# Optimization experiments

Hardware: AMD Instinct MI355X
Metric: run time of the kernel (lower is better)

Reference implementation:

```python
import jax, jax.numpy as jnp
import numpy as np
from jax import lax
import math

N_QUBITS = 10
N_LAYERS = 4
PI = jnp.float32(math.pi)


def _c(x):
    return x.astype(jnp.complex64)


def rx_mat(t):
    c = _c(jnp.cos(0.5 * t)); s = _c(jnp.sin(0.5 * t))
    return jnp.stack([jnp.stack([c, -1j * s]), jnp.stack([-1j * s, c])])


def ry_mat(t):
    c = _c(jnp.cos(0.5 * t)); s = _c(jnp.sin(0.5 * t))
    return jnp.stack([jnp.stack([c, -s]), jnp.stack([s, c])])


def rz_mat(t):
    e0 = jnp.exp(_c(jnp.zeros_like(t)) - 0.5j * _c(t))
    e1 = jnp.exp(0.5j * _c(t))
    z = jnp.zeros_like(e0)
    return jnp.stack([jnp.stack([e0, z]), jnp.stack([z, e1])])


def apply_1q(psi, U, q):
    # psi: (2,)*n complex, apply 2x2 U on axis q
    psi = jnp.moveaxis(psi, q, 0)
    psi = jnp.tensordot(U, psi, axes=(1, 0))
    return jnp.moveaxis(psi, 0, q)


def apply_cnot(psi, ctrl, tgt):
    psi = jnp.moveaxis(psi, (ctrl, tgt), (0, 1))
    a00, a01, a10, a11 = psi[0, 0], psi[0, 1], psi[1, 0], psi[1, 1]
    psi = jnp.stack([jnp.stack([a00, a01]), jnp.stack([a11, a10])])
    return jnp.moveaxis(psi, (0, 1), (ctrl, tgt))


def vqc(state, weights):
    # state: (D,) float32 angles; weights: (layers, n, 3)
    n, L = N_QUBITS, N_LAYERS
    D = state.shape[0]
    psi = jnp.full((2,) * n, 2.0 ** (-n / 2.0), dtype=jnp.complex64)  # H^n |0>
    for layer in range(L):
        for q in range(n):
            ang = state[(layer * n + q) % D]
            psi = apply_1q(psi, rx_mat(ang), q)
            psi = apply_1q(psi, ry_mat(ang), q)
            psi = apply_1q(psi, rz_mat(weights[layer, q, 0]), q)
            psi = apply_1q(psi, ry_mat(weights[layer, q, 1]), q)
            psi = apply_1q(psi, rz_mat(weights[layer, q, 2]), q)
        for q in range(n - 1):
            psi = apply_cnot(psi, q, q + 1)
        psi = apply_cnot(psi, n - 1, 0)
    probs = jnp.real(psi * jnp.conj(psi))  # (2,)*n
    zdiag = jnp.array([1.0, -1.0], dtype=jnp.float32)
    exps = [jnp.sum(probs * zdiag.reshape((1,) * q + (2,) + (1,) * (n - q - 1)))
            for q in range(n)]
    return jnp.stack(exps)  # (n,)


def lstm_forward(x, W_ih, W_hh, b_ih, b_hh):
    # x: [B,T,Din]; PyTorch gate order: i, f, g, o
    B, T, _ = x.shape
    H = W_hh.shape[1]
    b = b_ih + b_hh

    def step(carry, xt):
        h, c = carry
        gates = xt @ W_ih.T + h @ W_hh.T + b
        i, f, g, o = jnp.split(gates, 4, axis=-1)
        i = jax.nn.sigmoid(i); f = jax.nn.sigmoid(f)
        g = jnp.tanh(g); o = jax.nn.sigmoid(o)
        c = f * c + i * g
        h = o * jnp.tanh(c)
        return (h, c), h

    h0 = jnp.zeros((B, H), x.dtype)
    c0 = jnp.zeros((B, H), x.dtype)
    _, hs = lax.scan(step, (h0, c0), jnp.swapaxes(x, 0, 1))
    return jnp.swapaxes(hs, 0, 1)  # [B,T,H]


def _forward(s, lstm_s, W_ih, W_hh, b_ih, b_hh, proj_W, proj_b,
             in_proj_W, in_proj_b, out_proj_W, out_proj_b,
             qweights, W1, b1, W2, b2):
    hs = lstm_forward(lstm_s, W_ih, W_hh, b_ih, b_hh)      # [B,T,H]
    lstm_last = hs[:, -1, :]                               # [B,H]
    state_full = jnp.concatenate([lstm_last, s], axis=1)   # [B,E]
    lstm_proj = hs @ proj_W.T + proj_b                     # [B,T,E]
    E = proj_W.shape[0]
    Wq, Wk, Wv = in_proj_W[:E], in_proj_W[E:2 * E], in_proj_W[2 * E:]
    bq, bk, bv = in_proj_b[:E], in_proj_b[E:2 * E], in_proj_b[2 * E:]
    q = state_full @ Wq.T + bq                             # [B,E] (1 query token)
    k = lstm_proj @ Wk.T + bk                              # [B,T,E]
    v = lstm_proj @ Wv.T + bv
    scale = 1.0 / jnp.sqrt(jnp.float32(E))                 # num_heads=1 -> head_dim=E
    attn = jax.nn.softmax(jnp.einsum('be,bte->bt', q, k) * scale, axis=-1)
    ctx = jnp.einsum('bt,bte->be', attn, v)
    attn_out = ctx @ out_proj_W.T + out_proj_b             # [B,E]
    merged_state = jnp.concatenate([attn_out, s], axis=1)  # [B,E+F]
    state_norm = jnp.tanh(merged_state) * PI
    qfeat = jax.vmap(lambda st: vqc(st, qweights))(state_norm)  # [B,n]
    merged = jnp.concatenate([merged_state, qfeat], axis=1)
    x = jax.nn.relu(merged @ W1.T + b1)
    return x @ W2.T + b2


def setup_inputs() -> dict:
    key = jax.random.key(0)
    ks = jax.random.split(key, 16)
    B, T = 512, 256
    Din, H, F = 128, 256, 64
    E = H + F          # 320 = state_dim
    Dm = E + F         # 384 = merged_state dim
    n_l1, n_act = 512, 8

    def g(k, shape, std):
        return (std * jax.random.normal(k, shape)).astype(jnp.float32)

    return {
        's': jax.random.normal(ks[0], (B, F), jnp.float32),
        'lstm_s': jax.random.normal(ks[1], (B, T, Din), jnp.float32),
        'W_ih': g(ks[2], (4 * H, Din), 0.05),
        'W_hh': g(ks[3], (4 * H, H), 0.05),
        'b_ih': jnp.zeros((4 * H,), jnp.float32),
        'b_hh': jnp.zeros((4 * H,), jnp.float32),
        'proj_W': g(ks[4], (E, H), 0.05),
        'proj_b': 0.1 * jnp.ones((E,), jnp.float32),
        'in_proj_W': g(ks[5], (3 * E, E), 0.05),
        'in_proj_b': jnp.zeros((3 * E,), jnp.float32),
        'out_proj_W': g(ks[6], (E, E), 0.05),
        'out_proj_b': jnp.zeros((E,), jnp.float32),
        'qweights': jax.random.uniform(ks[7], (N_LAYERS, N_QUBITS, 3), jnp.float32, 0.0, 2.0 * math.pi),
        'W1': g(ks[8], (n_l1, Dm + N_QUBITS), 0.05),
        'b1': 0.1 * jnp.ones((n_l1,), jnp.float32),
        'W2': g(ks[9], (n_act, n_l1), 0.05),
        'b2': 0.1 * jnp.ones((n_act,), jnp.float32),
    }


def reference(s, lstm_s, W_ih, W_hh, b_ih, b_hh, proj_W, proj_b,
              in_proj_W, in_proj_b, out_proj_W, out_proj_b,
              qweights, W1, b1, W2, b2):
    return _forward(s, lstm_s, W_ih, W_hh, b_ih, b_hh, proj_W, proj_b,
                    in_proj_W, in_proj_b, out_proj_W, out_proj_b,
                    qweights, W1, b1, W2, b2)
```

## Files before the change

### kernel.cpp

```cpp
#include <hip/hip_runtime.h>
#include <hip/hip_bf16.h>
#include <math.h>

typedef unsigned int u32;
typedef unsigned long long u64;
typedef unsigned short u16;
typedef __attribute__((ext_vector_type(8))) short short8;
typedef __attribute__((ext_vector_type(4))) float f32x4;
typedef __attribute__((ext_vector_type(4))) int v4i;

#define PI_F 3.14159265358979f
#define B_   512
#define T_   256
#define DIN  128
#define H_   256
#define G4   1024
#define F_   64
#define E_   320
#define DM   384
#define NL1  512
#define NACT 8
#define KMLP 394

__device__ v4i llvm_amdgcn_raw_buffer_load_v4i32(v4i rsrc, int voffset,
                                                 int soffset, int aux)
    __asm("llvm.amdgcn.raw.buffer.load.v4i32");
__device__ void llvm_amdgcn_raw_buffer_store_i32(int vdata, v4i rsrc,
                                                 int voffset, int soffset,
                                                 int aux)
    __asm("llvm.amdgcn.raw.buffer.store.i32");

__device__ __forceinline__ v4i make_srd(const void* p) {
  v4i r;
  r.x = (int)(u32)(u64)p;
  r.y = (int)(u32)((u64)p >> 32);
  r.z = (int)0xFFFFFFFFu;
  r.w = 0x00020000;
  return r;
}

__device__ __forceinline__ float b2f(u16 h) {
  union { u32 u; float f; } v; v.u = ((u32)h) << 16; return v.f;
}
__device__ __forceinline__ u16 f2b(float f) {
  union { float f; u32 u; } v; v.f = f;
  u32 r = (v.u + 0x7FFFu + ((v.u >> 16) & 1u)) >> 16;
  return (u16)r;
}
__device__ __forceinline__ float sigf(float x) { return 1.0f / (1.0f + __expf(-x)); }
__device__ __forceinline__ float tanhfast(float x) { return 2.0f / (1.0f + __expf(-2.0f * x)) - 1.0f; }
__device__ __forceinline__ float2 cmul(float2 a, float2 b) {
  return make_float2(a.x * b.x - a.y * b.y, a.x * b.y + a.y * b.x);
}
__device__ __forceinline__ float2 cadd(float2 a, float2 b) {
  return make_float2(a.x + b.x, a.y + b.y);
}

__global__ void k_prep1(const float* __restrict__ lstm_s,
                        const float* __restrict__ W_ih,
                        const float* __restrict__ W_hh,
                        const float* __restrict__ b_ih,
                        const float* __restrict__ b_hh,
                        const float* __restrict__ ipw,
                        const float* __restrict__ ipb,
                        const float* __restrict__ projb,
                        const float* __restrict__ qw,
                        const float* __restrict__ W1,
                        u16* __restrict__ xbf,
                        u16* __restrict__ hs,
                        u16* __restrict__ Wg,
                        float* __restrict__ bb,
                        float* __restrict__ W1t,
                        float* __restrict__ uw,
                        float* __restrict__ bkp,
                        float* __restrict__ bvp,
                        u32* __restrict__ cnt) {
  const int bid = blockIdx.x;
  const int tid = threadIdx.x;
  if (bid < 8192) {
    u32 u = (u32)bid * 256u + tid;
    u32 c8 = u & 15u, b = (u >> 4) & 511u, t = u >> 13;
    const float* src = lstm_s + ((size_t)b * T_ + t) * DIN + c8 * 8;
    union { u16 h[8]; uint4 v; } tmp;
#pragma unroll
    for (int i = 0; i < 8; ++i) tmp.h[i] = f2b(src[i]);
    *(uint4*)(xbf + ((size_t)t * B_ + b) * DIN + c8 * 8) = tmp.v;
  } else if (bid < 8384) {
    u32 u = (u32)(bid - 8192) * 256u + tid;
    u32 c8 = u % 48u, r = u / 48u;
    const float* src = (c8 < 16) ? (W_ih + (size_t)r * DIN + c8 * 8)
                                 : (W_hh + (size_t)r * H_ + (c8 - 16) * 8);
    union { u16 h[8]; uint4 v; } tmp;
#pragma unroll
    for (int i = 0; i < 8; ++i) tmp.h[i] = f2b(src[i]);
    *(uint4*)(Wg + (size_t)r * 384 + c8 * 8) = tmp.v;
  } else if (bid < 8448) {
    u32 u = (u32)(bid - 8384) * 256u + tid;
    ((uint4*)hs)[u] = make_uint4(0, 0, 0, 0);
  } else if (bid < 9236) {
    u32 u = (u32)(bid - 8448) * 256u + tid;
    u32 k = u / 512u, nn = u % 512u;
    W1t[u] = W1[(size_t)nn * KMLP + k];
  } else if (bid == 9236) {
    for (int i = tid; i < 1024; i += 256) bb[i] = b_ih[i] + b_hh[i];
    for (int i = tid; i < 1024; i += 256) cnt[i] = 0u;
    if (tid < 40) {
      float w0 = qw[tid * 3 + 0], w1 = qw[tid * 3 + 1], w2 = qw[tid * 3 + 2];
      float c0 = cosf(0.5f * w0), s0 = sinf(0.5f * w0);
      float c1 = cosf(0.5f * w1), s1 = sinf(0.5f * w1);
      float c2 = cosf(0.5f * w2), s2 = sinf(0.5f * w2);
      float2 e0m = make_float2(c0, -s0), e0p = make_float2(c0, s0);
      float2 e2m = make_float2(c2, -s2), e2p = make_float2(c2, s2);
      float2 t00 = make_float2(c1 * e0m.x, c1 * e0m.y);
      float2 t01 = make_float2(-s1 * e0p.x, -s1 * e0p.y);
      float2 t10 = make_float2(s1 * e0m.x, s1 * e0m.y);
      float2 t11 = make_float2(c1 * e0p.x, c1 * e0p.y);
      float2 u00 = cmul(e2m, t00), u01 = cmul(e2m, t01);
      float2 u10 = cmul(e2p, t10), u11 = cmul(e2p, t11);
      float* o = uw + tid * 8;
      o[0] = u00.x; o[1] = u00.y; o[2] = u01.x; o[3] = u01.y;
      o[4] = u10.x; o[5] = u10.y; o[6] = u11.x; o[7] = u11.y;
    }
  } else if (bid <= 9238) {
    int o = (bid - 9237) * 256 + tid;
    if (o < E_) {
      float acc = ipb[E_ + o];
      for (int e = 0; e < E_; ++e) acc += ipw[(size_t)(E_ + o) * E_ + e] * projb[e];
      bkp[o] = acc;
    }
  } else {
    int o = (bid - 9239) * 256 + tid;
    if (o < E_) {
      float acc = ipb[2 * E_ + o];
      for (int e = 0; e < E_; ++e) acc += ipw[(size_t)(2 * E_ + o) * E_ + e] * projb[e];
      bvp[o] = acc;
    }
  }
}

__global__ void k_prep2(const float* __restrict__ ipw, const float* __restrict__ projW,
                        float* __restrict__ Wkp, float* __restrict__ Wvp) {
  int bid = blockIdx.x, tid = threadIdx.x;
  int o = (bid < 320) ? bid : (bid - 320);
  const float* wrow = ipw + (size_t)((bid < 320 ? E_ : 2 * E_) + o) * E_;
  float acc = 0.f;
  for (int e = 0; e < E_; ++e) acc += wrow[e] * projW[(size_t)e * H_ + tid];
  (bid < 320 ? Wkp : Wvp)[(size_t)o * H_ + tid] = acc;
}

__global__ void k_prep3(const float* __restrict__ ipw, const float* __restrict__ ipb,
                        const float* __restrict__ opw, const float* __restrict__ opb,
                        const float* __restrict__ Wkp, const float* __restrict__ Wvp,
                        const float* __restrict__ bkp, const float* __restrict__ bvp,
                        float* __restrict__ WuT, float* __restrict__ bu,
                        float* __restrict__ wd, float* __restrict__ ddp,
                        float* __restrict__ Wovt, float* __restrict__ bov) {
  int bid = blockIdx.x, tid = threadIdx.x;
  if (bid < 320) {
    int e = bid;
    float acc = 0.f;
    for (int o = 0; o < E_; ++o) acc += Wkp[(size_t)o * H_ + tid] * ipw[(size_t)o * E_ + e];
    WuT[(size_t)e * H_ + tid] = acc;
  } else if (bid < 576) {
    int jj = bid - 320;
    for (int i = tid; i < E_; i += 256) {
      float acc = 0.f;
      for (int o = 0; o < E_; ++o) acc += opw[(size_t)i * E_ + o] * Wvp[(size_t)o * H_ + jj];
      Wovt[(size_t)jj * E_ + i] = acc;
    }
  } else {
    {
      float acc = 0.f;
      for (int o = 0; o < E_; ++o) acc += Wkp[(size_t)o * H_ + tid] * ipb[o];
      bu[tid] = acc;
    }
    for (int idx = tid; idx < E_; idx += 256) {
      float a1 = 0.f, a2 = opb[idx];
      for (int o = 0; o < E_; ++o) {
        a1 += ipw[(size_t)o * E_ + idx] * bkp[o];
        a2 += opw[(size_t)idx * E_ + o] * bvp[o];
      }
      wd[idx] = a1; bov[idx] = a2;
    }
    if (tid == 0) {
      float acc = 0.f;
      for (int o = 0; o < E_; ++o) acc += ipb[o] * bkp[o];
      ddp[0] = acc;
    }
  }
}

struct LstmArgs {
  const u16* xbf; u16* hs; const u16* Wg; const float* bb; u32* cnt;
};

__launch_bounds__(256, 1)
__global__ void k_lstm(LstmArgs A) {
  const int g   = blockIdx.x & 7;
  const int n   = blockIdx.x >> 3;
  const int tid = threadIdx.x;
  const int wid = tid >> 6, lane = tid & 63;
  __shared__ __align__(16) u16 Wl[32 * 392];

  for (int idx = tid; idx < 32 * 48; idx += 256) {
    int ln = idx / 48, c8 = idx % 48;
    int gr = (ln >> 3) * 256 + n * 8 + (ln & 7);
    *(uint4*)&Wl[ln * 392 + c8 * 8] = *(const uint4*)&A.Wg[(size_t)gr * 384 + c8 * 8];
  }
  const int j  = lane & 7;
  const int gc = n * 8 + j;
  const float bbi = A.bb[gc], bbf2 = A.bb[256 + gc];
  const float bbg = A.bb[512 + gc], bbo = A.bb[768 + gc];

  const int quad = lane >> 4;
  const int mrow = lane & 15;
  const int brow = g * 64 + wid * 16 + mrow;
  const int erow0 = g * 64 + wid * 16 + quad * 4;
  const bool hi = (lane & 8) != 0;
  float crs[4] = {0.f, 0.f, 0.f, 0.f};
  u32* mycnt = A.cnt + g * 64;
  u32 target = 0;

  const v4i hs_srd = make_srd(A.hs);
  const int hvoff = (brow * H_ + quad * 8) * 2;

  uint4 xc0, xc1, xc2, xc3, xn0, xn1, xn2, xn3;
  {
    const u16* xb = A.xbf + ((size_t)0 * B_ + brow) * DIN + quad * 8;
    xc0 = *(const uint4*)(xb + 0);
    xc1 = *(const uint4*)(xb + 32);
    xc2 = *(const uint4*)(xb + 64);
    xc3 = *(const uint4*)(xb + 96);
  }
  __syncthreads();

  for (int t = 0; t < T_; ++t) {
    const int hsoff = t * (B_ * H_ * 2);
    uint4 h0 = __builtin_bit_cast(uint4, llvm_amdgcn_raw_buffer_load_v4i32(hs_srd, hvoff +   0, hsoff, 17));
    uint4 h1 = __builtin_bit_cast(uint4, llvm_amdgcn_raw_buffer_load_v4i32(hs_srd, hvoff +  64, hsoff, 17));
    uint4 h2 = __builtin_bit_cast(uint4, llvm_amdgcn_raw_buffer_load_v4i32(hs_srd, hvoff + 128, hsoff, 17));
    uint4 h3 = __builtin_bit_cast(uint4, llvm_amdgcn_raw_buffer_load_v4i32(hs_srd, hvoff + 192, hsoff, 17));
    uint4 h4 = __builtin_bit_cast(uint4, llvm_amdgcn_raw_buffer_load_v4i32(hs_srd, hvoff + 256, hsoff, 17));
    uint4 h5 = __builtin_bit_cast(uint4, llvm_amdgcn_raw_buffer_load_v4i32(hs_srd, hvoff + 320, hsoff, 17));
    uint4 h6 = __builtin_bit_cast(uint4, llvm_amdgcn_raw_buffer_load_v4i32(hs_srd, hvoff + 384, hsoff, 17));
    uint4 h7 = __builtin_bit_cast(uint4, llvm_amdgcn_raw_buffer_load_v4i32(hs_srd, hvoff + 448, hsoff, 17));
    {
      const int tn = (t + 1 < T_) ? (t + 1) : t;
      const u16* xb = A.xbf + ((size_t)tn * B_ + brow) * DIN + quad * 8;
      xn0 = *(const uint4*)(xb + 0);
      xn1 = *(const uint4*)(xb + 32);
      xn2 = *(const uint4*)(xb + 64);
      xn3 = *(const uint4*)(xb + 96);
    }

    f32x4 acc0 = {0.f, 0.f, 0.f, 0.f}, acc1 = {0.f, 0.f, 0.f, 0.f};
#define MMSTEP(AV, KOFF)                                                          \
    {                                                                             \
      short8 av  = __builtin_bit_cast(short8, AV);                                \
      short8 bv0 = __builtin_bit_cast(short8,                                     \
          *(const uint4*)&Wl[mrow * 392 + (KOFF) + quad * 8]);                    \
      short8 bv1 = __builtin_bit_cast(short8,                                     \
          *(const uint4*)&Wl[(16 + mrow) * 392 + (KOFF) + quad * 8]);             \
      acc0 = __builtin_amdgcn_mfma_f32_16x16x32_bf16(av, bv0, acc0, 0, 0, 0);     \
      acc1 = __builtin_amdgcn_mfma_f32_16x16x32_bf16(av, bv1, acc1, 0, 0, 0);     \
    }
    MMSTEP(xc0, 0)   MMSTEP(xc1, 32)  MMSTEP(xc2, 64)  MMSTEP(xc3, 96)
    MMSTEP(h0, 128)  MMSTEP(h1, 160)  MMSTEP(h2, 192)  MMSTEP(h3, 224)
    MMSTEP(h4, 256)  MMSTEP(h5, 288)  MMSTEP(h6, 320)  MMSTEP(h7, 352)
#undef MMSTEP

    const int hsoff_o = (t + 1) * (B_ * H_ * 2);
#pragma unroll
    for (int r = 0; r < 4; ++r) {
      float x0 = acc0[r], x1v = acc1[r];
      float y0 = __shfl_xor(x0, 8, 64);
      float y1 = __shfl_xor(x1v, 8, 64);
      float iv = (hi ? y0 : x0) + bbi;
      float fv = (hi ? x0 : y0) + bbf2;
      float gv = (hi ? y1 : x1v) + bbg;
      float ov = (hi ? x1v : y1) + bbo;
      float cc = sigf(fv) * crs[r] + sigf(iv) * tanhfast(gv);
      crs[r] = cc;
      float hh = sigf(ov) * tanhfast(cc);
      float hh2 = __shfl_xor(hh, 1, 64);
      if (!hi && ((j & 1) == 0)) {
        u32 pk = (u32)f2b(hh) | ((u32)f2b(hh2) << 16);
        llvm_amdgcn_raw_buffer_store_i32((int)pk, hs_srd,
                                         ((erow0 + r) * H_ + gc) * 2, hsoff_o, 17);
      }
    }
    target += 32;
    if (t != T_ - 1) {
      __syncthreads();
      if (tid == 0) {
        __hip_atomic_fetch_add(mycnt, 1u, __ATOMIC_RELAXED, __HIP_MEMORY_SCOPE_AGENT);
        int guard = 0;
        while (__hip_atomic_load(mycnt, __ATOMIC_RELAXED, __HIP_MEMORY_SCOPE_AGENT) < target) {
          __builtin_amdgcn_s_sleep(1);
          if (++guard > (1 << 24)) break;
        }
      }
      __syncthreads();
      xc0 = xn0; xc1 = xn1; xc2 = xn2; xc3 = xn3;
    }
  }
}

__global__ void k_u(const u16* __restrict__ hs, const float* __restrict__ s,
                    const float* __restrict__ WuT, const float* __restrict__ bu,
                    const float* __restrict__ wd, const float* __restrict__ ddp,
                    float* __restrict__ u, float* __restrict__ dvec) {
  int b = blockIdx.x, tid = threadIdx.x;
  __shared__ float z[E_];
  __shared__ float red[256];
  z[tid] = b2f(hs[((size_t)T_ * B_ + b) * H_ + tid]);
  if (tid < F_) z[H_ + tid] = s[(size_t)b * F_ + tid];
  __syncthreads();
  float acc = bu[tid];
  for (int e = 0; e < E_; ++e) acc += WuT[(size_t)e * H_ + tid] * z[e];
  u[(size_t)b * H_ + tid] = acc;
  float p = 0.f;
  for (int e = tid; e < E_; e += 256) p += wd[e] * z[e];
  red[tid] = p;
  __syncthreads();
  for (int s2 = 128; s2 > 0; s2 >>= 1) {
    if (tid < s2) red[tid] += red[tid + s2];
    __syncthreads();
  }
  if (tid == 0) dvec[b] = red[0] + ddp[0];
}

__global__ void k_aw(const u16* __restrict__ hs, const float* __restrict__ u,
                     const float* __restrict__ dvec, float* __restrict__ wv) {
  int b = blockIdx.x, tid = threadIdx.x;
  int wid = tid >> 6, lane = tid & 63;
  __shared__ float sc[T_];
  __shared__ float red[256];
  const float db = dvec[b];
  const float scale = 0.055901699437494745f;
  float4 ul = *(const float4*)&u[(size_t)b * H_ + lane * 4];
  for (int tt = 0; tt < 64; ++tt) {
    int t = wid * 64 + tt;
    u32 rw0 = ((const u32*)(hs + ((size_t)(t + 1) * B_ + b) * H_))[lane * 2];
    u32 rw1 = ((const u32*)(hs + ((size_t)(t + 1) * B_ + b) * H_))[lane * 2 + 1];
    union { u32 uu; float f; } f0, f1, f2, f3;
    f0.uu = rw0 << 16; f1.uu = rw0 & 0xFFFF0000u;
    f2.uu = rw1 << 16; f3.uu = rw1 & 0xFFFF0000u;
    float p = f0.f * ul.x + f1.f * ul.y + f2.f * ul.z + f3.f * ul.w;
#pragma unroll
    for (int off = 32; off > 0; off >>= 1) p += __shfl_xor(p, off, 64);
    if (lane == 0) sc[t] = (p + db) * scale;
  }
  __syncthreads();
  float v = sc[tid];
  red[tid] = v;
  __syncthreads();
  for (int s2 = 128; s2 > 0; s2 >>= 1) {
    if (tid < s2) red[tid] = fmaxf(red[tid], red[tid + s2]);
    __syncthreads();
  }
  float m = red[0];
  __syncthreads();
  float e = __expf(v - m);
  red[tid] = e;
  __syncthreads();
  for (int s2 = 128; s2 > 0; s2 >>= 1) {
    if (tid < s2) red[tid] += red[tid + s2];
    __syncthreads();
  }
  float inv = 1.f / red[0];
  __syncthreads();
  sc[tid] = e * inv;
  __syncthreads();
  float acc = 0.f;
#pragma unroll 8
  for (int t = 0; t < T_; ++t) {
    acc += sc[t] * b2f(hs[((size_t)(t + 1) * B_ + b) * H_ + tid]);
  }
  wv[(size_t)b * H_ + tid] = acc;
}

__global__ void k_ao(const float* __restrict__ wv, const float* __restrict__ Wovt,
                     const float* __restrict__ bov, const float* __restrict__ s,
                     float* __restrict__ mst) {
  int b = blockIdx.x, tid = threadIdx.x;
  __shared__ float wl[H_];
  if (tid < H_) wl[tid] = wv[(size_t)b * H_ + tid];
  __syncthreads();
  if (tid < E_) {
    float acc = bov[tid];
    for (int jj = 0; jj < H_; ++jj) acc += Wovt[(size_t)jj * E_ + tid] * wl[jj];
    mst[(size_t)b * DM + tid] = acc;
  } else if (tid < DM) {
    mst[(size_t)b * DM + tid] = s[(size_t)b * F_ + (tid - E_)];
  }
}

__global__ void k_vqc(const float* __restrict__ mst, const float* __restrict__ uwg,
                      float* __restrict__ qf) {
  int b = blockIdx.x, tid = threadIdx.x;
  __shared__ float2 psi[1024];
  __shared__ float ang[40];
  __shared__ float uwl[320];
  __shared__ float part[4][10];
  if (tid < 40) ang[tid] = tanhf(mst[(size_t)b * DM + tid]) * PI_F;
  uwl[tid] = uwg[tid];
  if (tid < 64) uwl[256 + tid] = uwg[256 + tid];
#pragma unroll
  for (int k = 0; k < 4; ++k) psi[tid + k * 256] = make_float2(0.03125f, 0.f);
  __syncthreads();
  for (int l = 0; l < 4; ++l) {
    for (int q = 0; q < 10; ++q) {
      int lq = l * 10 + q;
      float a = ang[lq];
      float ca = __cosf(0.5f * a), sa = __sinf(0.5f * a);
      float cs = ca * sa;
      float2 m00 = make_float2(ca * ca, sa * sa);
      float2 m01 = make_float2(-cs, -cs);
      float2 m10 = make_float2(cs, -cs);
      float2 m11 = make_float2(ca * ca, -sa * sa);
      const float* uwp = &uwl[lq * 8];
      float2 a00 = make_float2(uwp[0], uwp[1]), a01 = make_float2(uwp[2], uwp[3]);
      float2 a10 = make_float2(uwp[4], uwp[5]), a11 = make_float2(uwp[6], uwp[7]);
      float2 u00 = cadd(cmul(a00, m00), cmul(a01, m10));
      float2 u01 = cadd(cmul(a00, m01), cmul(a01, m11));
      float2 u10 = cadd(cmul(a10, m00), cmul(a11, m10));
      float2 u11 = cadd(cmul(a10, m01), cmul(a11, m11));
      int bp = 9 - q;
      __syncthreads();
#pragma unroll
      for (int k = 0; k < 2; ++k) {
        int p = tid + k * 256;
        int i0 = ((p >> bp) << (bp + 1)) | (p & ((1 << bp) - 1));
        int i1 = i0 | (1 << bp);
        float2 A0 = psi[i0], A1 = psi[i1];
        psi[i0] = cadd(cmul(u00, A0), cmul(u01, A1));
        psi[i1] = cadd(cmul(u10, A0), cmul(u11, A1));
      }
    }
    for (int q = 0; q < 9; ++q) {
      int lo = 8 - q;
      __syncthreads();
      int p = tid;
      int i0 = ((p >> lo) << (lo + 2)) | (2 << lo) | (p & ((1 << lo) - 1));
      int i1 = i0 | (1 << lo);
      float2 tmp = psi[i0]; psi[i0] = psi[i1]; psi[i1] = tmp;
    }
    __syncthreads();
    {
      int i0 = (tid << 1) | 1;
      int i1 = i0 | 512;
      float2 tmp = psi[i0]; psi[i0] = psi[i1]; psi[i1] = tmp;
    }
  }
  __syncthreads();
  float acc[10];
#pragma unroll
  for (int q = 0; q < 10; ++q) acc[q] = 0.f;
#pragma unroll
  for (int k = 0; k < 4; ++k) {
    int idx = tid + k * 256;
    float2 A = psi[idx];
    float pr = A.x * A.x + A.y * A.y;
#pragma unroll
    for (int q = 0; q < 10; ++q) acc[q] += ((idx >> (9 - q)) & 1) ? -pr : pr;
  }
  int lane = tid & 63, wid = tid >> 6;
#pragma unroll
  for (int q = 0; q < 10; ++q) {
    float vq = acc[q];
#pragma unroll
    for (int off = 32; off > 0; off >>= 1) vq += __shfl_xor(vq, off, 64);
    if (lane == 0) part[wid][q] = vq;
  }
  __syncthreads();
  if (tid < 10) qf[(size_t)b * 10 + tid] = part[0][tid] + part[1][tid] + part[2][tid] + part[3][tid];
}

__global__ void k_mlp(const float* __restrict__ mst, const float* __restrict__ qf,
                      const float* __restrict__ W1t, const float* __restrict__ b1,
                      const float* __restrict__ W2, const float* __restrict__ b2,
                      float* __restrict__ out) {
  int b = blockIdx.x, tid = threadIdx.x;
  __shared__ float mg[KMLP];
  __shared__ float x1[NL1];
  __shared__ float red[256];
  for (int i = tid; i < DM; i += 256) mg[i] = mst[(size_t)b * DM + i];
  if (tid < 10) mg[DM + tid] = qf[(size_t)b * 10 + tid];
  __syncthreads();
#pragma unroll
  for (int hh = 0; hh < 2; ++hh) {
    int nn = tid + hh * 256;
    float acc = b1[nn];
#pragma unroll 4
    for (int k = 0; k < KMLP; ++k) acc += W1t[(size_t)k * NL1 + nn] * mg[k];
    x1[nn] = fmaxf(acc, 0.f);
  }
  __syncthreads();
  int a = tid >> 5, l32 = tid & 31;
  float p = 0.f;
  for (int k = l32; k < NL1; k += 32) p += x1[k] * W2[(size_t)a * NL1 + k];
  red[tid] = p;
  __syncthreads();
  if (tid < 8) {
    float acc = b2[tid];
#pragma unroll
    for (int i = 0; i < 32; ++i) acc += red[tid * 32 + i];
    out[(size_t)b * NACT + tid] = acc;
  }
}

extern "C" void kernel_launch(void* const* d_in, const int* in_sizes, int n_in,
                              void* d_out, int out_size, void* d_ws, size_t ws_size,
                              hipStream_t stream) {
  const float* s      = (const float*)d_in[0];
  const float* lstm_s = (const float*)d_in[1];
  const float* W_ih   = (const float*)d_in[2];
  const float* W_hh   = (const float*)d_in[3];
  const float* b_ih   = (const float*)d_in[4];
  const float* b_hh   = (const float*)d_in[5];
  const float* projW  = (const float*)d_in[6];
  const float* projb  = (const float*)d_in[7];
  const float* ipw    = (const float*)d_in[8];
  const float* ipb    = (const float*)d_in[9];
  const float* opw    = (const float*)d_in[10];
  const float* opb    = (const float*)d_in[11];
  const float* qw     = (const float*)d_in[12];
  const float* W1     = (const float*)d_in[13];
  const float* b1     = (const float*)d_in[14];
  const float* W2     = (const float*)d_in[15];
  const float* b2     = (const float*)d_in[16];
  float* out = (float*)d_out;

  char* wsb = (char*)d_ws;
  size_t off = 0;
  auto alloc = [&](size_t bytes) -> void* {
    void* p = wsb + off;
    off = (off + bytes + 255) & ~(size_t)255;
    return p;
  };
  u16*  xbf  = (u16*)alloc((size_t)T_ * B_ * DIN * 2);
  u16*  hs   = (u16*)alloc((size_t)(T_ + 1) * B_ * H_ * 2);
  u16*  Wg   = (u16*)alloc((size_t)G4 * 384 * 2);
  float* bb  = (float*)alloc(G4 * 4);
  float* Wkp = (float*)alloc((size_t)E_ * H_ * 4);
  float* Wvp = (float*)alloc((size_t)E_ * H_ * 4);
  float* bkp = (float*)alloc(E_ * 4);
  float* bvp = (float*)alloc(E_ * 4);
  float* WuT = (float*)alloc((size_t)E_ * H_ * 4);
  float* bu  = (float*)alloc(H_ * 4);
  float* wd  = (float*)alloc(E_ * 4);
  float* ddp = (float*)alloc(256);
  float* Wovt= (float*)alloc((size_t)H_ * E_ * 4);
  float* bov = (float*)alloc(E_ * 4);
  float* uu  = (float*)alloc((size_t)B_ * H_ * 4);
  float* dvec= (float*)alloc(B_ * 4);
  float* wv  = (float*)alloc((size_t)B_ * H_ * 4);
  float* mst = (float*)alloc((size_t)B_ * DM * 4);
  float* qf  = (float*)alloc((size_t)B_ * 10 * 4);
  float* uw  = (float*)alloc(40 * 8 * 4);
  float* W1t = (float*)alloc((size_t)KMLP * NL1 * 4);
  u32*  cnt  = (u32*)alloc(1024 * 4);
  (void)ws_size; (void)in_sizes; (void)n_in; (void)out_size;

  hipLaunchKernelGGL(k_prep1, dim3(9241), dim3(256), 0, stream,
                     lstm_s, W_ih, W_hh, b_ih, b_hh, ipw, ipb, projb, qw, W1,
                     xbf, hs, Wg, bb, W1t, uw, bkp, bvp, cnt);
  hipLaunchKernelGGL(k_prep2, dim3(640), dim3(256), 0, stream, ipw, projW, Wkp, Wvp);
  hipLaunchKernelGGL(k_prep3, dim3(577), dim3(256), 0, stream,
                     ipw, ipb, opw, opb, Wkp, Wvp, bkp, bvp, WuT, bu, wd, ddp, Wovt, bov);

  LstmArgs la;
  la.xbf = xbf; la.hs = hs; la.Wg = Wg; la.bb = bb; la.cnt = cnt;
  void* kargs[] = { (void*)&la };
  hipError_t ce = hipLaunchCooperativeKernel(reinterpret_cast<const void*>(&k_lstm),
                                             dim3(256), dim3(256), kargs, 0, stream);
  if (ce != hipSuccess) {
    hipLaunchKernelGGL(k_lstm, dim3(256), dim3(256), 0, stream, la);
  }

  hipLaunchKernelGGL(k_u,   dim3(512), dim3(256), 0, stream, hs, s, WuT, bu, wd, ddp, uu, dvec);
  hipLaunchKernelGGL(k_aw,  dim3(512), dim3(256), 0, stream, hs, uu, dvec, wv);
  hipLaunchKernelGGL(k_ao,  dim3(512), dim3(384), 0, stream, wv, Wovt, bov, s, mst);
  hipLaunchKernelGGL(k_vqc, dim3(512), dim3(256), 0, stream, mst, uw, qf);
  hipLaunchKernelGGL(k_mlp, dim3(512), dim3(256), 0, stream, mst, qf, W1t, b1, W2, b2, out);
}
```

Before: 1.333 ms.

## Fuse post-LSTM attention, projection, VQC and MLP kernels into one per-batch kernel

Merges the five per-sample kernels that run after the LSTM (query projection, attention softmax and weighted sum, output projection, quantum circuit simulation, MLP head) into one kernel with one block per batch row. Intermediates stay in shared memory instead of going through global buffers, and four launches are removed. In exchange, k_ao's 384-thread block becomes a 256-thread loop, and the larger shared memory footprint per block may lower occupancy.

```diff
diff --git a/kernel.cpp b/kernel.cpp
--- a/kernel.cpp
+++ b/kernel.cpp
@@ -306,207 +306,205 @@
   }
 }
 
-__global__ void k_u(const u16* __restrict__ hs, const float* __restrict__ s,
-                    const float* __restrict__ WuT, const float* __restrict__ bu,
-                    const float* __restrict__ wd, const float* __restrict__ ddp,
-                    float* __restrict__ u, float* __restrict__ dvec) {
+__global__ void k_post(const u16* __restrict__ hs, const float* __restrict__ s,
+                       const float* __restrict__ WuT, const float* __restrict__ bu,
+                       const float* __restrict__ wd, const float* __restrict__ ddp,
+                       const float* __restrict__ Wovt, const float* __restrict__ bov,
+                       const float* __restrict__ uwg,
+                       const float* __restrict__ W1t, const float* __restrict__ b1,
+                       const float* __restrict__ W2, const float* __restrict__ b2,
+                       float* __restrict__ out) {
   int b = blockIdx.x, tid = threadIdx.x;
+  int wid = tid >> 6, lane = tid & 63;
   __shared__ float z[E_];
   __shared__ float red[256];
-  z[tid] = b2f(hs[((size_t)T_ * B_ + b) * H_ + tid]);
-  if (tid < F_) z[H_ + tid] = s[(size_t)b * F_ + tid];
-  __syncthreads();
-  float acc = bu[tid];
-  for (int e = 0; e < E_; ++e) acc += WuT[(size_t)e * H_ + tid] * z[e];
-  u[(size_t)b * H_ + tid] = acc;
-  float p = 0.f;
-  for (int e = tid; e < E_; e += 256) p += wd[e] * z[e];
-  red[tid] = p;
-  __syncthreads();
-  for (int s2 = 128; s2 > 0; s2 >>= 1) {
-    if (tid < s2) red[tid] += red[tid + s2];
-    __syncthreads();
-  }
-  if (tid == 0) dvec[b] = red[0] + ddp[0];
-}
-
-__global__ void k_aw(const u16* __restrict__ hs, const float* __restrict__ u,
-                     const float* __restrict__ dvec, float* __restrict__ wv) {
-  int b = blockIdx.x, tid = threadIdx.x;
-  int wid = tid >> 6, lane = tid & 63;
+  __shared__ float ul_s[H_];
   __shared__ float sc[T_];
-  __shared__ float red[256];
-  const float db = dvec[b];
-  const float scale = 0.055901699437494745f;
-  float4 ul = *(const float4*)&u[(size_t)b * H_ + lane * 4];
-  for (int tt = 0; tt < 64; ++tt) {
-    int t = wid * 64 + tt;
-    u32 rw0 = ((const u32*)(hs + ((size_t)(t + 1) * B_ + b) * H_))[lane * 2];
-    u32 rw1 = ((const u32*)(hs + ((size_t)(t + 1) * B_ + b) * H_))[lane * 2 + 1];
-    union { u32 uu; float f; } f0, f1, f2, f3;
-    f0.uu = rw0 << 16; f1.uu = rw0 & 0xFFFF0000u;
-    f2.uu = rw1 << 16; f3.uu = rw1 & 0xFFFF0000u;
-    float p = f0.f * ul.x + f1.f * ul.y + f2.f * ul.z + f3.f * ul.w;
-#pragma unroll
-    for (int off = 32; off > 0; off >>= 1) p += __shfl_xor(p, off, 64);
-    if (lane == 0) sc[t] = (p + db) * scale;
-  }
-  __syncthreads();
-  float v = sc[tid];
-  red[tid] = v;
-  __syncthreads();
-  for (int s2 = 128; s2 > 0; s2 >>= 1) {
-    if (tid < s2) red[tid] = fmaxf(red[tid], red[tid + s2]);
-    __syncthreads();
-  }
-  float m = red[0];
-  __syncthreads();
-  float e = __expf(v - m);
-  red[tid] = e;
-  __syncthreads();
-  for (int s2 = 128; s2 > 0; s2 >>= 1) {
-    if (tid < s2) red[tid] += red[tid + s2];
-    __syncthreads();
-  }
-  float inv = 1.f / red[0];
-  __syncthreads();
-  sc[tid] = e * inv;
-  __syncthreads();
-  float acc = 0.f;
-#pragma unroll 8
-  for (int t = 0; t < T_; ++t) {
-    acc += sc[t] * b2f(hs[((size_t)(t + 1) * B_ + b) * H_ + tid]);
-  }
-  wv[(size_t)b * H_ + tid] = acc;
-}
-
-__global__ void k_ao(const float* __restrict__ wv, const float* __restrict__ Wovt,
-                     const float* __restrict__ bov, const float* __restrict__ s,
-                     float* __restrict__ mst) {
-  int b = blockIdx.x, tid = threadIdx.x;
-  __shared__ float wl[H_];
-  if (tid < H_) wl[tid] = wv[(size_t)b * H_ + tid];
-  __syncthreads();
-  if (tid < E_) {
-    float acc = bov[tid];
-    for (int jj = 0; jj < H_; ++jj) acc += Wovt[(size_t)jj * E_ + tid] * wl[jj];
-    mst[(size_t)b * DM + tid] = acc;
-  } else if (tid < DM) {
-    mst[(size_t)b * DM + tid] = s[(size_t)b * F_ + (tid - E_)];
-  }
-}
-
-__global__ void k_vqc(const float* __restrict__ mst, const float* __restrict__ uwg,
-                      float* __restrict__ qf) {
-  int b = blockIdx.x, tid = threadIdx.x;
+  __shared__ float wv_s[H_];
+  __shared__ float mst_l[DM];
+  __shared__ float dvec_s;
   __shared__ float2 psi[1024];
   __shared__ float ang[40];
   __shared__ float uwl[320];
   __shared__ float part[4][10];
-  if (tid < 40) ang[tid] = tanhf(mst[(size_t)b * DM + tid]) * PI_F;
-  uwl[tid] = uwg[tid];
-  if (tid < 64) uwl[256 + tid] = uwg[256 + tid];
-#pragma unroll
-  for (int k = 0; k < 4; ++k) psi[tid + k * 256] = make_float2(0.03125f, 0.f);
-  __syncthreads();
-  for (int l = 0; l < 4; ++l) {
-    for (int q = 0; q < 10; ++q) {
-      int lq = l * 10 + q;
-      float a = ang[lq];
-      float ca = __cosf(0.5f * a), sa = __sinf(0.5f * a);
-      float cs = ca * sa;
-      float2 m00 = make_float2(ca * ca, sa * sa);
-      float2 m01 = make_float2(-cs, -cs);
-      float2 m10 = make_float2(cs, -cs);
-      float2 m11 = make_float2(ca * ca, -sa * sa);
-      const float* uwp = &uwl[lq * 8];
-      float2 a00 = make_float2(uwp[0], uwp[1]), a01 = make_float2(uwp[2], uwp[3]);
-      float2 a10 = make_float2(uwp[4], uwp[5]), a11 = make_float2(uwp[6], uwp[7]);
-      float2 u00 = cadd(cmul(a00, m00), cmul(a01, m10));
-      float2 u01 = cadd(cmul(a00, m01), cmul(a01, m11));
-      float2 u10 = cadd(cmul(a10, m00), cmul(a11, m10));
-      float2 u11 = cadd(cmul(a10, m01), cmul(a11, m11));
-      int bp = 9 - q;
-      __syncthreads();
-#pragma unroll
-      for (int k = 0; k < 2; ++k) {
-        int p = tid + k * 256;
-        int i0 = ((p >> bp) << (bp + 1)) | (p & ((1 << bp) - 1));
-        int i1 = i0 | (1 << bp);
-        float2 A0 = psi[i0], A1 = psi[i1];
-        psi[i0] = cadd(cmul(u00, A0), cmul(u01, A1));
-        psi[i1] = cadd(cmul(u10, A0), cmul(u11, A1));
-      }
-    }
-    for (int q = 0; q < 9; ++q) {
-      int lo = 8 - q;
-      __syncthreads();
-      int p = tid;
-      int i0 = ((p >> lo) << (lo + 2)) | (2 << lo) | (p & ((1 << lo) - 1));
-      int i1 = i0 | (1 << lo);
-      float2 tmp = psi[i0]; psi[i0] = psi[i1]; psi[i1] = tmp;
-    }
-    __syncthreads();
-    {
-      int i0 = (tid << 1) | 1;
-      int i1 = i0 | 512;
-      float2 tmp = psi[i0]; psi[i0] = psi[i1]; psi[i1] = tmp;
-    }
-  }
-  __syncthreads();
-  float acc[10];
-#pragma unroll
-  for (int q = 0; q < 10; ++q) acc[q] = 0.f;
-#pragma unroll
-  for (int k = 0; k < 4; ++k) {
-    int idx = tid + k * 256;
-    float2 A = psi[idx];
-    float pr = A.x * A.x + A.y * A.y;
-#pragma unroll
-    for (int q = 0; q < 10; ++q) acc[q] += ((idx >> (9 - q)) & 1) ? -pr : pr;
-  }
-  int lane = tid & 63, wid = tid >> 6;
-#pragma unroll
-  for (int q = 0; q < 10; ++q) {
-    float vq = acc[q];
-#pragma unroll
-    for (int off = 32; off > 0; off >>= 1) vq += __shfl_xor(vq, off, 64);
-    if (lane == 0) part[wid][q] = vq;
-  }
-  __syncthreads();
-  if (tid < 10) qf[(size_t)b * 10 + tid] = part[0][tid] + part[1][tid] + part[2][tid] + part[3][tid];
-}
-
-__global__ void k_mlp(const float* __restrict__ mst, const float* __restrict__ qf,
-                      const float* __restrict__ W1t, const float* __restrict__ b1,
-                      const float* __restrict__ W2, const float* __restrict__ b2,
-                      float* __restrict__ out) {
-  int b = blockIdx.x, tid = threadIdx.x;
+  __shared__ float qf_s[10];
   __shared__ float mg[KMLP];
   __shared__ float x1[NL1];
-  __shared__ float red[256];
-  for (int i = tid; i < DM; i += 256) mg[i] = mst[(size_t)b * DM + i];
-  if (tid < 10) mg[DM + tid] = qf[(size_t)b * 10 + tid];
+
+  z[tid] = b2f(hs[((size_t)T_ * B_ + b) * H_ + tid]);
+  if (tid < F_) z[H_ + tid] = s[(size_t)b * F_ + tid];
   __syncthreads();
-#pragma unroll
-  for (int hh = 0; hh < 2; ++hh) {
-    int nn = tid + hh * 256;
-    float acc = b1[nn];
+  {
+    float acc = bu[tid];
+    for (int e = 0; e < E_; ++e) acc += WuT[(size_t)e * H_ + tid] * z[e];
+    ul_s[tid] = acc;
+    float p = 0.f;
+    for (int e = tid; e < E_; e += 256) p += wd[e] * z[e];
+    red[tid] = p;
+    __syncthreads();
+    for (int s2 = 128; s2 > 0; s2 >>= 1) {
+      if (tid < s2) red[tid] += red[tid + s2];
+      __syncthreads();
+    }
+    if (tid == 0) dvec_s = red[0] + ddp[0];
+    __syncthreads();
+  }
+
+  {
+    const float db = dvec_s;
+    const float scale = 0.055901699437494745f;
+    float4 ul = make_float4(ul_s[lane * 4], ul_s[lane * 4 + 1],
+                            ul_s[lane * 4 + 2], ul_s[lane * 4 + 3]);
+    for (int tt = 0; tt < 64; ++tt) {
+      int t = wid * 64 + tt;
+      u32 rw0 = ((const u32*)(hs + ((size_t)(t + 1) * B_ + b) * H_))[lane * 2];
+      u32 rw1 = ((const u32*)(hs + ((size_t)(t + 1) * B_ + b) * H_))[lane * 2 + 1];
+      union { u32 uu; float f; } f0, f1, f2, f3;
+      f0.uu = rw0 << 16; f1.uu = rw0 & 0xFFFF0000u;
+      f2.uu = rw1 << 16; f3.uu = rw1 & 0xFFFF0000u;
+      float p = f0.f * ul.x + f1.f * ul.y + f2.f * ul.z + f3.f * ul.w;
+#pragma unroll
+      for (int off = 32; off > 0; off >>= 1) p += __shfl_xor(p, off, 64);
+      if (lane == 0) sc[t] = (p + db) * scale;
+    }
+    __syncthreads();
+    float v = sc[tid];
+    red[tid] = v;
+    __syncthreads();
+    for (int s2 = 128; s2 > 0; s2 >>= 1) {
+      if (tid < s2) red[tid] = fmaxf(red[tid], red[tid + s2]);
+      __syncthreads();
+    }
+    float m = red[0];
+    __syncthreads();
+    float e = __expf(v - m);
+    red[tid] = e;
+    __syncthreads();
+    for (int s2 = 128; s2 > 0; s2 >>= 1) {
+      if (tid < s2) red[tid] += red[tid + s2];
+      __syncthreads();
+    }
+    float inv = 1.f / red[0];
+    __syncthreads();
+    sc[tid] = e * inv;
+    __syncthreads();
+    float acc = 0.f;
+#pragma unroll 8
+    for (int t = 0; t < T_; ++t) {
+      acc += sc[t] * b2f(hs[((size_t)(t + 1) * B_ + b) * H_ + tid]);
+    }
+    wv_s[tid] = acc;
+    __syncthreads();
+  }
+
+  {
+    for (int i = tid; i < E_; i += 256) {
+      float acc = bov[i];
+      for (int jj = 0; jj < H_; ++jj) acc += Wovt[(size_t)jj * E_ + i] * wv_s[jj];
+      mst_l[i] = acc;
+    }
+    if (tid < F_) mst_l[E_ + tid] = s[(size_t)b * F_ + tid];
+    __syncthreads();
+  }
+
+  {
+    if (tid < 40) ang[tid] = tanhf(mst_l[tid]) * PI_F;
+    uwl[tid] = uwg[tid];
+    if (tid < 64) uwl[256 + tid] = uwg[256 + tid];
+#pragma unroll
+    for (int k = 0; k < 4; ++k) psi[tid + k * 256] = make_float2(0.03125f, 0.f);
+    __syncthreads();
+    for (int l = 0; l < 4; ++l) {
+      for (int q = 0; q < 10; ++q) {
+        int lq = l * 10 + q;
+        float a = ang[lq];
+        float ca = __cosf(0.5f * a), sa = __sinf(0.5f * a);
+        float cs = ca * sa;
+        float2 m00 = make_float2(ca * ca, sa * sa);
+        float2 m01 = make_float2(-cs, -cs);
+        float2 m10 = make_float2(cs, -cs);
+        float2 m11 = make_float2(ca * ca, -sa * sa);
+        const float* uwp = &uwl[lq * 8];
+        float2 a00 = make_float2(uwp[0], uwp[1]), a01 = make_float2(uwp[2], uwp[3]);
+        float2 a10 = make_float2(uwp[4], uwp[5]), a11 = make_float2(uwp[6], uwp[7]);
+        float2 u00 = cadd(cmul(a00, m00), cmul(a01, m10));
+        float2 u01 = cadd(cmul(a00, m01), cmul(a01, m11));
+        float2 u10 = cadd(cmul(a10, m00), cmul(a11, m10));
+        float2 u11 = cadd(cmul(a10, m01), cmul(a11, m11));
+        int bp = 9 - q;
+        __syncthreads();
+#pragma unroll
+        for (int k = 0; k < 2; ++k) {
+          int p = tid + k * 256;
+          int i0 = ((p >> bp) << (bp + 1)) | (p & ((1 << bp) - 1));
+          int i1 = i0 | (1 << bp);
+          float2 A0 = psi[i0], A1 = psi[i1];
+          psi[i0] = cadd(cmul(u00, A0), cmul(u01, A1));
+          psi[i1] = cadd(cmul(u10, A0), cmul(u11, A1));
+        }
+      }
+      for (int q = 0; q < 9; ++q) {
+        int lo = 8 - q;
+        __syncthreads();
+        int p = tid;
+        int i0 = ((p >> lo) << (lo + 2)) | (2 << lo) | (p & ((1 << lo) - 1));
+        int i1 = i0 | (1 << lo);
+        float2 tmp = psi[i0]; psi[i0] = psi[i1]; psi[i1] = tmp;
+      }
+      __syncthreads();
+      {
+        int i0 = (tid << 1) | 1;
+        int i1 = i0 | 512;
+        float2 tmp = psi[i0]; psi[i0] = psi[i1]; psi[i1] = tmp;
+      }
+    }
+    __syncthreads();
+    float acc[10];
+#pragma unroll
+    for (int q = 0; q < 10; ++q) acc[q] = 0.f;
+#pragma unroll
+    for (int k = 0; k < 4; ++k) {
+      int idx = tid + k * 256;
+      float2 A = psi[idx];
+      float pr = A.x * A.x + A.y * A.y;
+#pragma unroll
+      for (int q = 0; q < 10; ++q) acc[q] += ((idx >> (9 - q)) & 1) ? -pr : pr;
+    }
+#pragma unroll
+    for (int q = 0; q < 10; ++q) {
+      float vq = acc[q];
+#pragma unroll
+      for (int off = 32; off > 0; off >>= 1) vq += __shfl_xor(vq, off, 64);
+      if (lane == 0) part[wid][q] = vq;
+    }
+    __syncthreads();
+    if (tid < 10) qf_s[tid] = part[0][tid] + part[1][tid] + part[2][tid] + part[3][tid];
+  }
+
+  {
+    for (int i = tid; i < DM; i += 256) mg[i] = mst_l[i];
+    if (tid < 10) mg[DM + tid] = qf_s[tid];
+    __syncthreads();
+#pragma unroll
+    for (int hh = 0; hh < 2; ++hh) {
+      int nn = tid + hh * 256;
+      float acc = b1[nn];
 #pragma unroll 4
-    for (int k = 0; k < KMLP; ++k) acc += W1t[(size_t)k * NL1 + nn] * mg[k];
-    x1[nn] = fmaxf(acc, 0.f);
-  }
-  __syncthreads();
-  int a = tid >> 5, l32 = tid & 31;
-  float p = 0.f;
-  for (int k = l32; k < NL1; k += 32) p += x1[k] * W2[(size_t)a * NL1 + k];
-  red[tid] = p;
-  __syncthreads();
-  if (tid < 8) {
-    float acc = b2[tid];
-#pragma unroll
-    for (int i = 0; i < 32; ++i) acc += red[tid * 32 + i];
-    out[(size_t)b * NACT + tid] = acc;
+      for (int k = 0; k < KMLP; ++k) acc += W1t[(size_t)k * NL1 + nn] * mg[k];
+      x1[nn] = fmaxf(acc, 0.f);
+    }
+    __syncthreads();
+    int a = tid >> 5, l32 = tid & 31;
+    float p = 0.f;
+    for (int k = l32; k < NL1; k += 32) p += x1[k] * W2[(size_t)a * NL1 + k];
+    red[tid] = p;
+    __syncthreads();
+    if (tid < 8) {
+      float acc = b2[tid];
+#pragma unroll
+      for (int i = 0; i < 32; ++i) acc += red[tid * 32 + i];
+      out[(size_t)b * NACT + tid] = acc;
+    }
   }
 }
 
@@ -553,11 +551,6 @@
   float* ddp = (float*)alloc(256);
   float* Wovt= (float*)alloc((size_t)H_ * E_ * 4);
   float* bov = (float*)alloc(E_ * 4);
-  float* uu  = (float*)alloc((size_t)B_ * H_ * 4);
-  float* dvec= (float*)alloc(B_ * 4);
-  float* wv  = (float*)alloc((size_t)B_ * H_ * 4);
-  float* mst = (float*)alloc((size_t)B_ * DM * 4);
-  float* qf  = (float*)alloc((size_t)B_ * 10 * 4);
   float* uw  = (float*)alloc(40 * 8 * 4);
   float* W1t = (float*)alloc((size_t)KMLP * NL1 * 4);
   u32*  cnt  = (u32*)alloc(1024 * 4);
@@ -579,9 +572,6 @@
     hipLaunchKernelGGL(k_lstm, dim3(256), dim3(256), 0, stream, la);
   }
 
-  hipLaunchKernelGGL(k_u,   dim3(512), dim3(256), 0, stream, hs, s, WuT, bu, wd, ddp, uu, dvec);
-  hipLaunchKernelGGL(k_aw,  dim3(512), dim3(256), 0, stream, hs, uu, dvec, wv);
-  hipLaunchKernelGGL(k_ao,  dim3(512), dim3(384), 0, stream, wv, Wovt, bov, s, mst);
-  hipLaunchKernelGGL(k_vqc, dim3(512), dim3(256), 0, stream, mst, uw, qf);
-  hipLaunchKernelGGL(k_mlp, dim3(512), dim3(256), 0, stream, mst, qf, W1t, b1, W2, b2, out);
-}
+  hipLaunchKernelGGL(k_post, dim3(512), dim3(256), 0, stream,
+                     hs, s, WuT, bu, wd, ddp, Wovt, bov, uw, W1t, b1, W2, b2, out);
+}
```

Result: faster. 1.295 ms (-2.9%).
